# Kernel optimization log

Hardware: AMD Instinct MI355X
Metric: run time of the kernel (lower is better)

Reference implementation:

```python
import jax, jax.numpy as jnp
import numpy as np

N = 8192
IN_F = 256
OUT_F = 128
ALPHA = 0.2  # leakyrelu slope
NEG_BIG = -9e15


def setup_inputs() -> dict:
    key = jax.random.key(0)
    k1, k2, k3, k4 = jax.random.split(key, 4)
    x = jax.random.normal(k1, (N, IN_F), dtype=jnp.float32)
    adj = (jax.random.uniform(k2, (N, N)) < 0.01).astype(jnp.float32)
    adj = jnp.maximum(adj, jnp.eye(N, dtype=jnp.float32))
    # xavier-uniform-style init scales
    W = jax.random.uniform(k3, (IN_F, OUT_F), dtype=jnp.float32,
                           minval=-1.0, maxval=1.0) * np.sqrt(6.0 / (IN_F + OUT_F))
    a = jax.random.uniform(k4, (2 * OUT_F, 1), dtype=jnp.float32,
                           minval=-1.0, maxval=1.0) * np.sqrt(6.0 / (2 * OUT_F + 1))
    return {"x": x, "adj": adj, "W": W, "a": a}


def reference(x, adj, W, a):
    # h = x @ W  -> (N, F)
    h = x @ W
    # e_ij = leakyrelu(a^T [h_i || h_j]) = leakyrelu((h @ a1)_i + (h @ a2)_j)
    # equivalent to torch's repeat/cat construction, without the N^2*2F tensor
    a1 = a[:OUT_F, 0]   # (F,)
    a2 = a[OUT_F:, 0]   # (F,)
    s1 = h @ a1         # (N,)
    s2 = h @ a2         # (N,)
    e = s1[:, None] + s2[None, :]                      # (N, N)
    e = jnp.where(e > 0, e, ALPHA * e)                 # leakyrelu
    att = jnp.where(adj > 0, e, NEG_BIG)
    att = jax.nn.softmax(att, axis=1)                  # (N, N)
    # dropout is identity in eval mode
    h_prime = att @ h                                  # (N, F)
    return jax.nn.elu(h_prime)
```

## Files before the change

### kernel.cpp

```cpp
#include <hip/hip_runtime.h>
#include <cstdint>
#include <cstddef>

#define N 8192
#define IN_F 256
#define OUT_F 128
#define ALPHA 0.2f
#define CAP 256
typedef unsigned long long ull;
typedef float f32x4 __attribute__((ext_vector_type(4)));

__device__ __forceinline__ float bf2f(unsigned short u) {
    return __uint_as_float(((unsigned)u) << 16);
}
__device__ __forceinline__ unsigned short f2bf(float f) {
    unsigned x = __float_as_uint(f);
    unsigned r = (x + 0x7FFFu + ((x >> 16) & 1u)) >> 16;
    return (unsigned short)r;
}

__global__ __launch_bounds__(256) void gemm_xw(const float* __restrict__ x,
                                               const float* __restrict__ W,
                                               const float* __restrict__ a,
                                               unsigned short* __restrict__ hb,
                                               float* __restrict__ s1,
                                               float* __restrict__ s2) {
    __shared__ __align__(16) float xsT[64 * 20];
    __shared__ __align__(16) float ws[64 * 128];
    const int tid = threadIdx.x;
    const int R0  = blockIdx.x * 16;
    const int r0  = (tid >> 5) * 2;
    const int c0  = (tid & 31) * 4;

    float acc[2][4];
#pragma unroll
    for (int r = 0; r < 2; ++r)
#pragma unroll
        for (int c = 0; c < 4; ++c) acc[r][c] = 0.f;

    for (int k0 = 0; k0 < IN_F; k0 += 64) {
        {
            const int r  = tid >> 4;
            const int k4 = tid & 15;
            const float4 v = *(const float4*)(x + (size_t)(R0 + r) * IN_F + k0 + k4 * 4);
            xsT[(k4 * 4 + 0) * 20 + r] = v.x;
            xsT[(k4 * 4 + 1) * 20 + r] = v.y;
            xsT[(k4 * 4 + 2) * 20 + r] = v.z;
            xsT[(k4 * 4 + 3) * 20 + r] = v.w;
        }
#pragma unroll
        for (int q = 0; q < 8; ++q) {
            const int f = tid + q * 256;
            *(float4*)(ws + f * 4) = *(const float4*)(W + (size_t)k0 * OUT_F + f * 4);
        }
        __syncthreads();

#pragma unroll 8
        for (int kk = 0; kk < 64; ++kk) {
            const float4 wv = *(const float4*)(ws + kk * 128 + c0);
            const float2 xv = *(const float2*)(xsT + kk * 20 + r0);
            acc[0][0] += xv.x * wv.x; acc[0][1] += xv.x * wv.y; acc[0][2] += xv.x * wv.z; acc[0][3] += xv.x * wv.w;
            acc[1][0] += xv.y * wv.x; acc[1][1] += xv.y * wv.y; acc[1][2] += xv.y * wv.z; acc[1][3] += xv.y * wv.w;
        }
        __syncthreads();
    }

#pragma unroll
    for (int r = 0; r < 2; ++r) {
        ushort4 o4;
        o4.x = f2bf(acc[r][0]); o4.y = f2bf(acc[r][1]);
        o4.z = f2bf(acc[r][2]); o4.w = f2bf(acc[r][3]);
        *(ushort4*)(hb + (size_t)(R0 + r0 + r) * OUT_F + c0) = o4;
    }

    const float4 a1v = *(const float4*)(a + c0);
    const float4 a2v = *(const float4*)(a + OUT_F + c0);
#pragma unroll
    for (int r = 0; r < 2; ++r) {
        float p1 = acc[r][0] * a1v.x + acc[r][1] * a1v.y + acc[r][2] * a1v.z + acc[r][3] * a1v.w;
        float p2 = acc[r][0] * a2v.x + acc[r][1] * a2v.y + acc[r][2] * a2v.z + acc[r][3] * a2v.w;
#pragma unroll
        for (int off = 16; off > 0; off >>= 1) {
            p1 += __shfl_xor(p1, off);
            p2 += __shfl_xor(p2, off);
        }
        if ((tid & 31) == 0) {
            s1[R0 + r0 + r] = p1;
            s2[R0 + r0 + r] = p2;
        }
    }
}

__global__ __launch_bounds__(256, 8) void gat_fused(const float* __restrict__ adj,
                                                    const unsigned short* __restrict__ hb,
                                                    const float* __restrict__ s1,
                                                    const float* __restrict__ s2,
                                                    float* __restrict__ out) {
    const int tid  = threadIdx.x;
    const int wv   = tid >> 6;
    const int lane = tid & 63;
    const int row  = blockIdx.x * 4 + wv;

    __shared__ int   jl[4][CAP];
    __shared__ float el[4][CAP];

    const f32x4* __restrict__ arow = (const f32x4*)(adj + (size_t)row * N);
    const ull below = (1ull << lane) - 1ull;

    int tot = 0;
    f32x4 buf[8];
#pragma unroll
    for (int u = 0; u < 8; ++u) buf[u] = arow[lane + u * 64];

#pragma unroll
    for (int g = 0; g < 4; ++g) {
#pragma unroll
        for (int u = 0; u < 8; ++u) {
            const f32x4 v = buf[u];
            if (g < 3) buf[u] = arow[lane + ((g + 1) * 8 + u) * 64];
            const int jb = (((g * 8 + u) * 64) + lane) * 4;
            const float av[4] = {v.x, v.y, v.z, v.w};
#pragma unroll
            for (int c = 0; c < 4; ++c) {
                const bool hit = av[c] > 0.f;
                const ull m = __ballot(hit);
                if (m) {
                    const int base = tot;
                    tot += __popcll(m);
                    if (hit) {
                        const int p = base + __popcll(m & below);
                        if (p < CAP) jl[wv][p] = jb + c;
                    }
                }
            }
        }
    }
    const int n = tot < CAP ? tot : CAP;

    const float si = s1[row];
    float ev[4];
    float lmax = -1e30f;
#pragma unroll
    for (int t = 0; t < 4; ++t) {
        const int l = lane + t * 64;
        float e = -1e30f;
        if (l < n) {
            e = si + s2[jl[wv][l]];
            e = e > 0.f ? e : ALPHA * e;
        }
        ev[t] = e;
        lmax = fmaxf(lmax, e);
    }
#pragma unroll
    for (int off = 32; off > 0; off >>= 1) lmax = fmaxf(lmax, __shfl_xor(lmax, off));

    float dp = 0.f;
#pragma unroll
    for (int t = 0; t < 4; ++t) {
        const int l = lane + t * 64;
        if (l < n) {
            const float wgt = __expf(ev[t] - lmax);
            el[wv][l] = wgt;
            dp += wgt;
        }
    }
#pragma unroll
    for (int off = 32; off > 0; off >>= 1) dp += __shfl_xor(dp, off);
    const float denom = dp;

    const int half = lane >> 5;
    const int col4 = (lane & 31) * 4;
    float a0 = 0.f, a1 = 0.f, a2 = 0.f, a3 = 0.f;
#pragma unroll 4
    for (int l = half; l < n; l += 2) {
        const float wgt = el[wv][l];
        const int j = jl[wv][l];
        const ushort4 hv = *(const ushort4*)(hb + (size_t)j * OUT_F + col4);
        a0 += wgt * bf2f(hv.x);
        a1 += wgt * bf2f(hv.y);
        a2 += wgt * bf2f(hv.z);
        a3 += wgt * bf2f(hv.w);
    }
    a0 += __shfl_xor(a0, 32);
    a1 += __shfl_xor(a1, 32);
    a2 += __shfl_xor(a2, 32);
    a3 += __shfl_xor(a3, 32);

    if (half == 0) {
        const float r = 1.f / denom;
        float v0 = a0 * r, v1 = a1 * r, v2 = a2 * r, v3 = a3 * r;
        float4 o;
        o.x = v0 > 0.f ? v0 : (__expf(v0) - 1.f);
        o.y = v1 > 0.f ? v1 : (__expf(v1) - 1.f);
        o.z = v2 > 0.f ? v2 : (__expf(v2) - 1.f);
        o.w = v3 > 0.f ? v3 : (__expf(v3) - 1.f);
        *(float4*)(out + (size_t)row * OUT_F + col4) = o;
    }
}

extern "C" void kernel_launch(void* const* d_in, const int* in_sizes, int n_in,
                              void* d_out, int out_size, void* d_ws, size_t ws_size,
                              hipStream_t stream) {
    const float* x   = (const float*)d_in[0];
    const float* adj = (const float*)d_in[1];
    const float* W   = (const float*)d_in[2];
    const float* a   = (const float*)d_in[3];
    float* out = (float*)d_out;

    char* wsb = (char*)d_ws;
    unsigned short* hb = (unsigned short*)wsb;
    float* s1 = (float*)(wsb + 2 * 1024 * 1024);
    float* s2 = s1 + N;

    gemm_xw<<<N / 16, 256, 0, stream>>>(x, W, a, hb, s1, s2);
    gat_fused<<<2048, 256, 0, stream>>>(adj, hb, s1, s2, out);
}
```

Baseline: 71.17 us.

## Stream adjacency scan directly into online weighted aggregation without neighbor list

Replaces the two-phase approach (compact neighbor indices into shared memory, then softmax and gather) with a single pass. For each ballot hit it computes the attention weight and accumulates the bf16 feature row immediately, with each lane owning two output columns. s2 is staged in shared memory per block, and blocks grow to 8 waves. The max subtraction is dropped, so exp of unnormalized logits risks overflow for larger scores. The per-hit gather is also serialized inside the adjacency scan, which may reduce memory-level parallelism.

```diff
diff --git a/kernel.cpp b/kernel.cpp
--- a/kernel.cpp
+++ b/kernel.cpp
@@ -6,7 +6,6 @@
 #define IN_F 256
 #define OUT_F 128
 #define ALPHA 0.2f
-#define CAP 256
 typedef unsigned long long ull;
 typedef float f32x4 __attribute__((ext_vector_type(4)));
 
@@ -91,111 +90,70 @@
     }
 }
 
-__global__ __launch_bounds__(256, 8) void gat_fused(const float* __restrict__ adj,
-                                                    const unsigned short* __restrict__ hb,
+__global__ __launch_bounds__(512, 8) void gat_fused(const float* __restrict__ adj,
+                                                    const unsigned* __restrict__ hb32,
                                                     const float* __restrict__ s1,
                                                     const float* __restrict__ s2,
                                                     float* __restrict__ out) {
     const int tid  = threadIdx.x;
     const int wv   = tid >> 6;
     const int lane = tid & 63;
-    const int row  = blockIdx.x * 4 + wv;
+    const int row  = blockIdx.x * 8 + wv;
 
-    __shared__ int   jl[4][CAP];
-    __shared__ float el[4][CAP];
-
-    const f32x4* __restrict__ arow = (const f32x4*)(adj + (size_t)row * N);
-    const ull below = (1ull << lane) - 1ull;
-
-    int tot = 0;
-    f32x4 buf[8];
-#pragma unroll
-    for (int u = 0; u < 8; ++u) buf[u] = arow[lane + u * 64];
+    __shared__ __align__(16) float s2l[N];
 
 #pragma unroll
-    for (int g = 0; g < 4; ++g) {
+    for (int q = 0; q < 4; ++q) {
+        const int idx = tid + q * 512;
+        *(float4*)(s2l + idx * 4) = *(const float4*)(s2 + idx * 4);
+    }
+    __syncthreads();
+
+    const float si = s1[row];
+    const f32x4* __restrict__ arow = (const f32x4*)(adj + (size_t)row * N);
+
+    float acc0 = 0.f, acc1 = 0.f, dp = 0.f;
+
+    f32x4 va[4], vb[4];
 #pragma unroll
-        for (int u = 0; u < 8; ++u) {
-            const f32x4 v = buf[u];
-            if (g < 3) buf[u] = arow[lane + ((g + 1) * 8 + u) * 64];
-            const int jb = (((g * 8 + u) * 64) + lane) * 4;
-            const float av[4] = {v.x, v.y, v.z, v.w};
+    for (int u = 0; u < 4; ++u) va[u] = arow[lane + u * 64];
+
+    for (int b = 0; b < 8; ++b) {
+        if (b < 7) {
+#pragma unroll
+            for (int u = 0; u < 4; ++u) vb[u] = arow[lane + ((b + 1) * 4 + u) * 64];
+        }
+#pragma unroll
+        for (int u = 0; u < 4; ++u) {
+            const int base = (b * 4 + u) * 256;
+            const float av[4] = {va[u].x, va[u].y, va[u].z, va[u].w};
 #pragma unroll
             for (int c = 0; c < 4; ++c) {
-                const bool hit = av[c] > 0.f;
-                const ull m = __ballot(hit);
-                if (m) {
-                    const int base = tot;
-                    tot += __popcll(m);
-                    if (hit) {
-                        const int p = base + __popcll(m & below);
-                        if (p < CAP) jl[wv][p] = jb + c;
-                    }
+                ull m = __ballot(av[c] > 0.f);
+                while (m) {
+                    const int bt = __builtin_ctzll(m);
+                    m &= m - 1;
+                    const int j = base + 4 * bt + c;
+                    float e = si + s2l[j];
+                    e = e > 0.f ? e : ALPHA * e;
+                    const float w = __expf(e);
+                    const unsigned hv = hb32[j * 64 + lane];
+                    acc0 += w * bf2f((unsigned short)(hv & 0xFFFFu));
+                    acc1 += w * bf2f((unsigned short)(hv >> 16));
+                    dp += w;
                 }
             }
         }
+#pragma unroll
+        for (int u = 0; u < 4; ++u) va[u] = vb[u];
     }
-    const int n = tot < CAP ? tot : CAP;
 
-    const float si = s1[row];
-    float ev[4];
-    float lmax = -1e30f;
-#pragma unroll
-    for (int t = 0; t < 4; ++t) {
-        const int l = lane + t * 64;
-        float e = -1e30f;
-        if (l < n) {
-            e = si + s2[jl[wv][l]];
-            e = e > 0.f ? e : ALPHA * e;
-        }
-        ev[t] = e;
-        lmax = fmaxf(lmax, e);
-    }
-#pragma unroll
-    for (int off = 32; off > 0; off >>= 1) lmax = fmaxf(lmax, __shfl_xor(lmax, off));
-
-    float dp = 0.f;
-#pragma unroll
-    for (int t = 0; t < 4; ++t) {
-        const int l = lane + t * 64;
-        if (l < n) {
-            const float wgt = __expf(ev[t] - lmax);
-            el[wv][l] = wgt;
-            dp += wgt;
-        }
-    }
-#pragma unroll
-    for (int off = 32; off > 0; off >>= 1) dp += __shfl_xor(dp, off);
-    const float denom = dp;
-
-    const int half = lane >> 5;
-    const int col4 = (lane & 31) * 4;
-    float a0 = 0.f, a1 = 0.f, a2 = 0.f, a3 = 0.f;
-#pragma unroll 4
-    for (int l = half; l < n; l += 2) {
-        const float wgt = el[wv][l];
-        const int j = jl[wv][l];
-        const ushort4 hv = *(const ushort4*)(hb + (size_t)j * OUT_F + col4);
-        a0 += wgt * bf2f(hv.x);
-        a1 += wgt * bf2f(hv.y);
-        a2 += wgt * bf2f(hv.z);
-        a3 += wgt * bf2f(hv.w);
-    }
-    a0 += __shfl_xor(a0, 32);
-    a1 += __shfl_xor(a1, 32);
-    a2 += __shfl_xor(a2, 32);
-    a3 += __shfl_xor(a3, 32);
-
-    if (half == 0) {
-        const float r = 1.f / denom;
-        float v0 = a0 * r, v1 = a1 * r, v2 = a2 * r, v3 = a3 * r;
-        float4 o;
-        o.x = v0 > 0.f ? v0 : (__expf(v0) - 1.f);
-        o.y = v1 > 0.f ? v1 : (__expf(v1) - 1.f);
-        o.z = v2 > 0.f ? v2 : (__expf(v2) - 1.f);
-        o.w = v3 > 0.f ? v3 : (__expf(v3) - 1.f);
-        *(float4*)(out + (size_t)row * OUT_F + col4) = o;
-    }
+    const float r = 1.f / dp;
+    float v0 = acc0 * r, v1 = acc1 * r;
+    float2 o;
+    o.x = v0 > 0.f ? v0 : (__expf(v0) - 1.f);
+    o.y = v1 > 0.f ? v1 : (__expf(v1) - 1.f);
+    *(float2*)(out + (size_t)row * OUT_F + 2 * lane) = o;
 }
 
 extern "C" void kernel_launch(void* const* d_in, const int* in_sizes, int n_in,
@@ -213,5 +171,5 @@
     float* s2 = s1 + N;
 
     gemm_xw<<<N / 16, 256, 0, stream>>>(x, W, a, hb, s1, s2);
-    gat_fused<<<2048, 256, 0, stream>>>(adj, hb, s1, s2, out);
+    gat_fused<<<1024, 512, 0, stream>>>(adj, (const unsigned*)hb, s1, s2, out);
 }
```

Result: slower. 81.62 us (+14.7%).
